# Optimization experiments

Measured on AMD Instinct MI355X. Metric: run time of the kernel, lower is better.

Reference implementation:

```python
import jax, jax.numpy as jnp
import numpy as np

CAPACITY = 0.5  # top_k = int(seq_len * capacity)

def setup_inputs() -> dict:
    key = jax.random.key(0)
    k1, k2, k3, k4 = jax.random.split(key, 4)
    b, s, d, d_ff = 4, 4096, 1024, 4096
    x = jax.random.normal(k1, (b, s, d), dtype=jnp.float32)
    mask = jnp.ones((b, s), dtype=jnp.bool_)
    # learned params: router (Linear(d,1,bias=False)) and the block MLP
    Wr = jax.random.normal(k2, (d, 1), dtype=jnp.float32) * (d ** -0.5)
    W1 = jax.random.normal(k3, (d, d_ff), dtype=jnp.float32) * (d ** -0.5)
    W2 = jax.random.normal(k4, (d_ff, d), dtype=jnp.float32) * (d_ff ** -0.5)
    return {"x": x, "mask": mask, "Wr": Wr, "W1": W1, "W2": W2}

def reference(x, mask, Wr, W1, W2):
    b, s, d = x.shape
    top_k = int(s * CAPACITY)
    # router logits [b, s]
    logits = (x @ Wr)[..., 0]
    # top-k over sequence dim (torch sorted=False; softmax/gather are
    # permutation-equivariant so sorted top_k gives identical results)
    vals, idx = jax.lax.top_k(logits, top_k)          # [b, k]
    order = jnp.argsort(idx, axis=1)                  # sort selected indices ascending
    sel = jnp.take_along_axis(idx, order, axis=1)     # [b, k] token positions, ascending
    w = jax.nn.softmax(vals, axis=1)                  # softmax over selected logits
    r_w = jnp.take_along_axis(w, order, axis=1)       # weights reordered to match sel
    # gather selected tokens
    fx = jnp.take_along_axis(x, sel[..., None], axis=1)  # [b, k, d]
    # block: residual MLP whose update is scaled by router weights (mask unused by MLP)
    h = jax.nn.silu(fx @ W1) @ W2
    out = fx + h * r_w[..., None]
    # scatter processed tokens back into x
    batch = jnp.arange(b)[:, None]
    hidden_states = x.at[batch, sel].set(out)
    # aux loss: faithful to the original (flat view + flat index set, then BCE-with-logits mean)
    flat_logits = logits.reshape(-1)                  # [b*s]
    targets = jnp.zeros_like(flat_logits).at[sel.reshape(-1)].set(1.0)
    aux_loss = jnp.mean(
        jnp.maximum(flat_logits, 0.0)
        - flat_logits * targets
        + jnp.log1p(jnp.exp(-jnp.abs(flat_logits)))
    )
    return hidden_states, aux_loss
```

## Files before the change

kernel.cpp:

```cpp
#include <hip/hip_runtime.h>
#include <hip/hip_bf16.h>
#include <cstdint>

#define B_ 4
#define S_ 4096
#define D_ 1024
#define DFF_ 4096
#define KSEL_ 2048
#define M_ (B_ * KSEL_)
#define NTOK_ (B_ * S_)

typedef short bf16x8 __attribute__((ext_vector_type(8)));
typedef float f32x4 __attribute__((ext_vector_type(4)));

__device__ inline unsigned short f2bf(float f) {
    union { float f; unsigned int u; } c; c.f = f;
    unsigned int u = c.u;
    unsigned int r = u + 0x7fffu + ((u >> 16) & 1u);
    return (unsigned short)(r >> 16);
}

__global__ __launch_bounds__(256)
void transpose_bf16(const float* __restrict__ src, unsigned short* __restrict__ dst,
                    int R, int C) {
    __shared__ float tile[32][33];
    int c0 = blockIdx.x * 32, r0 = blockIdx.y * 32;
    for (int i = threadIdx.y; i < 32; i += 8)
        tile[i][threadIdx.x] = src[(size_t)(r0 + i) * C + c0 + threadIdx.x];
    __syncthreads();
    for (int i = threadIdx.y; i < 32; i += 8)
        dst[(size_t)(c0 + i) * R + r0 + threadIdx.x] = f2bf(tile[threadIdx.x][i]);
}

__global__ __launch_bounds__(256)
void router_kernel(const float* __restrict__ x, const float* __restrict__ Wr,
                   float* __restrict__ logits, unsigned short* __restrict__ xb,
                   float* __restrict__ out) {
    int wid = threadIdx.x >> 6, lane = threadIdx.x & 63;
    int row = blockIdx.x * 4 + wid;
    const float* xr = x + (size_t)row * D_;
    unsigned short* xbr = xb + (size_t)row * D_;
    float* outr = out + (size_t)row * D_;
    float acc = 0.f;
#pragma unroll
    for (int j = 0; j < 4; j++) {
        int off = j * 256 + lane * 4;
        float4 v = *(const float4*)(xr + off);
        float4 w = *(const float4*)(Wr + off);
        acc += v.x * w.x + v.y * w.y + v.z * w.z + v.w * w.w;
        *(float4*)(outr + off) = v;
        ushort4 o;
        o.x = f2bf(v.x); o.y = f2bf(v.y); o.z = f2bf(v.z); o.w = f2bf(v.w);
        *(ushort4*)(xbr + off) = o;
    }
#pragma unroll
    for (int s = 32; s; s >>= 1) acc += __shfl_xor(acc, s);
    if (lane == 0) logits[row] = acc;
}

__global__ __launch_bounds__(256)
void rank_partial_kernel(const float* __restrict__ logits, int* __restrict__ rank) {
    __shared__ float lj[512];
    int b  = blockIdx.x >> 7;
    int ic = (blockIdx.x >> 3) & 15;
    int jc = blockIdx.x & 7;
    const float* L = logits + b * S_;
    for (int t = threadIdx.x; t < 512; t += 256) lj[t] = L[jc * 512 + t];
    __syncthreads();
    int i = ic * 256 + threadIdx.x;
    float li = L[i];
    int jbase = jc * 512;
    int r = 0;
    const float4* __restrict__ lj4 = (const float4*)lj;
#pragma unroll 4
    for (int q = 0; q < 128; q++) {
        float4 v = lj4[q];
        int jb = jbase + q * 4;
        r += (v.x > li) | ((v.x == li) & (jb     < i));
        r += (v.y > li) | ((v.y == li) & (jb + 1 < i));
        r += (v.z > li) | ((v.z == li) & (jb + 2 < i));
        r += (v.w > li) | ((v.w == li) & (jb + 3 < i));
    }
    atomicAdd(&rank[b * S_ + i], r);
}

__global__ __launch_bounds__(256)
void compact_kernel(const float* __restrict__ logits, const int* __restrict__ rank,
                    int* __restrict__ flags,
                    int* __restrict__ rowidx, float* __restrict__ rw) {
    __shared__ float lg[S_];
    __shared__ int f[S_];
    __shared__ int tsum[256];
    __shared__ float red[256];
    int b = blockIdx.x;
    const float* L = logits + b * S_;
    const int* R = rank + b * S_;
    int* F = flags + b * S_;
    for (int j = threadIdx.x; j < S_ / 4; j += 256) {
        ((float4*)lg)[j] = ((const float4*)L)[j];
        int4 rk = ((const int4*)R)[j];
        int4 fl;
        fl.x = rk.x < KSEL_; fl.y = rk.y < KSEL_;
        fl.z = rk.z < KSEL_; fl.w = rk.w < KSEL_;
        ((int4*)f)[j] = fl;
        ((int4*)F)[j] = fl;
    }
    __syncthreads();
    float mx = -INFINITY;
    for (int j = threadIdx.x; j < S_; j += 256) mx = fmaxf(mx, lg[j]);
    red[threadIdx.x] = mx; __syncthreads();
    for (int s = 128; s; s >>= 1) {
        if (threadIdx.x < s) red[threadIdx.x] = fmaxf(red[threadIdx.x], red[threadIdx.x + s]);
        __syncthreads();
    }
    float m = red[0];
    __syncthreads();

    float esum = 0.f;
    int s0 = 0;
#pragma unroll
    for (int j = 0; j < 16; j++) {
        int i = threadIdx.x * 16 + j;
        s0 += f[i];
        if (f[i]) esum += expf(lg[i] - m);
    }
    red[threadIdx.x] = esum; __syncthreads();
    for (int s = 128; s; s >>= 1) {
        if (threadIdx.x < s) red[threadIdx.x] += red[threadIdx.x + s];
        __syncthreads();
    }
    float inv = 1.f / red[0];

    tsum[threadIdx.x] = s0; __syncthreads();
    for (int s = 1; s < 256; s <<= 1) {
        int u = (threadIdx.x >= s) ? tsum[threadIdx.x - s] : 0;
        __syncthreads();
        tsum[threadIdx.x] += u;
        __syncthreads();
    }
    int pos = tsum[threadIdx.x] - s0;
    for (int j = 0; j < 16; j++) {
        int i = threadIdx.x * 16 + j;
        if (f[i]) {
            rowidx[b * KSEL_ + pos] = b * S_ + i;
            rw[b * KSEL_ + pos] = expf(lg[i] - m) * inv;
            pos++;
        }
    }
}

__global__ __launch_bounds__(256)
void loss_kernel(const float* __restrict__ logits, const int* __restrict__ flags,
                 float* __restrict__ partials) {
    __shared__ float red[256];
    int i = blockIdx.x * 256 + threadIdx.x;
    float l = logits[i];
    float t = 0.f;
    if (i < S_)
        t = (flags[i] | flags[S_ + i] | flags[2 * S_ + i] | flags[3 * S_ + i]) ? 1.f : 0.f;
    float v = fmaxf(l, 0.f) - l * t + log1pf(expf(-fabsf(l)));
    red[threadIdx.x] = v; __syncthreads();
    for (int s = 128; s; s >>= 1) {
        if (threadIdx.x < s) red[threadIdx.x] += red[threadIdx.x + s];
        __syncthreads();
    }
    if (threadIdx.x == 0) partials[blockIdx.x] = red[0];
}

__global__ void loss_final(const float* __restrict__ partials, float* __restrict__ out) {
    float v = partials[threadIdx.x];
#pragma unroll
    for (int s = 32; s; s >>= 1) v += __shfl_xor(v, s);
    if (threadIdx.x == 0) out[0] = v / (float)NTOK_;
}

template <int MODE, int N, int K, int SUBS>
__global__ __launch_bounds__(512, 2)
void gemm_pipe_kernel(const unsigned short* __restrict__ A,
                      const unsigned short* __restrict__ BT,
                      const int* __restrict__ rowidx,
                      const float* __restrict__ rw,
                      const float* __restrict__ x,
                      unsigned short* __restrict__ Hout,
                      float* __restrict__ Out) {
    constexpr int BM = 128, BN = 256, BK = 64;
    constexpr int KI = K / BK;
    constexpr int NT = N / BN;
    constexpr int MG = M_ / (BM * SUBS);
    constexpr int NWG = NT * MG;
    constexpr int CPX = NWG / 8;
    __shared__ __attribute__((aligned(16))) unsigned short As[3][BM * BK];
    __shared__ __attribute__((aligned(16))) unsigned short Bs[3][BN * BK];

    const int tid = threadIdx.x;
    const int w = tid >> 6, lane = tid & 63;
    const int wm = w >> 2, wn = w & 3;

    int wgid = blockIdx.y * NT + blockIdx.x;
    int swz = (wgid & 7) * CPX + (wgid >> 3);
    const int tile_n = (swz % NT) * BN;
    const int mgrp   = (swz / NT);

    const int srow = lane >> 3;
    const int sw = (lane & 7) ^ srow;
    const uint64_t abase = (uint64_t)(uintptr_t)A;
    const uint64_t bbase = (uint64_t)(uintptr_t)BT;
    uint64_t aaddr[SUBS][2], baddr[4];
#pragma unroll
    for (int s = 0; s < SUBS; ++s)
#pragma unroll
        for (int t = 0; t < 2; ++t) {
            int r = t * 64 + w * 8 + srow;
            int am = (mgrp * SUBS + s) * BM + r;
            int ar = (MODE == 1) ? rowidx[am] : am;
            aaddr[s][t] = abase + ((uint64_t)ar * K + (uint64_t)sw * 8) * 2ull;
        }
#pragma unroll
    for (int t = 0; t < 4; ++t) {
        int r = t * 64 + w * 8 + srow;
        baddr[t] = bbase + ((uint64_t)(tile_n + r) * K + (uint64_t)sw * 8) * 2ull;
    }

    auto gload = [&](unsigned short* lds, uint64_t gaddr) {
        __builtin_amdgcn_global_load_lds(
            (const __attribute__((address_space(1))) unsigned int*)(uintptr_t)gaddr,
            (__attribute__((address_space(3))) unsigned int*)lds, 16, 0, 0);
    };

    f32x4 acc[4][4];
#pragma unroll
    for (int i = 0; i < 4; i++)
#pragma unroll
        for (int j = 0; j < 4; j++) acc[i][j] = (f32x4){0.f, 0.f, 0.f, 0.f};

#pragma unroll
    for (int p = 0; p < 2; ++p) {
        const uint64_t koff = (uint64_t)p * (BK * 2);
        gload(&As[p][(0 * 64 + w * 8) * BK], aaddr[0][0] + koff);
        gload(&As[p][(1 * 64 + w * 8) * BK], aaddr[0][1] + koff);
#pragma unroll
        for (int t = 0; t < 4; ++t)
            gload(&Bs[p][(t * 64 + w * 8) * BK], baddr[t] + koff);
    }
    asm volatile("s_waitcnt vmcnt(6)" ::: "memory");
    asm volatile("s_barrier" ::: "memory");

    const int lr = lane & 15, quad = lane >> 4;
    int c = 0;
#pragma unroll
    for (int s = 0; s < SUBS; ++s) {
#pragma unroll 1
        for (int kt = 0; kt < KI; ++kt) {
            int pre = c + 2; if (pre >= 3) pre -= 3;
            const char* Abase_l = (const char*)&As[c][0];
            const char* Bbase_l = (const char*)&Bs[c][0];
            const bool cross = (kt + 2 >= KI);
            const bool do_stage = (s < SUBS - 1) || (kt + 2 < KI);
            const uint64_t sa0 = cross ? aaddr[(s + 1 < SUBS) ? s + 1 : s][0]
                                       : aaddr[s][0];
            const uint64_t sa1 = cross ? aaddr[(s + 1 < SUBS) ? s + 1 : s][1]
                                       : aaddr[s][1];
            const uint64_t koff = (uint64_t)((kt + 2) & (KI - 1)) * (BK * 2);

            {
                bf16x8 af[4], bfr[4];
                const int xo = (quad ^ (lr & 7)) * 16;
#pragma unroll
                for (int m4 = 0; m4 < 4; ++m4) {
                    int row = wm * 64 + m4 * 16 + lr;
                    af[m4] = *(const bf16x8*)(Abase_l + row * (BK * 2) + xo);
                }
#pragma unroll
                for (int n4 = 0; n4 < 4; ++n4) {
                    int col = wn * 64 + n4 * 16 + lr;
                    bfr[n4] = *(const bf16x8*)(Bbase_l + col * (BK * 2) + xo);
                }
                if (do_stage) {
                    gload(&As[pre][(0 * 64 + w * 8) * BK], sa0 + koff);
                    gload(&As[pre][(1 * 64 + w * 8) * BK], sa1 + koff);
                    gload(&Bs[pre][(w * 8) * BK], baddr[0] + koff);
                }
                asm volatile("s_barrier" ::: "memory");
                asm volatile("s_waitcnt lgkmcnt(0)" ::: "memory");
                __builtin_amdgcn_sched_barrier(0);
                __builtin_amdgcn_s_setprio(1);
#pragma unroll
                for (int m4 = 0; m4 < 4; ++m4)
#pragma unroll
                    for (int n4 = 0; n4 < 4; ++n4)
                        acc[m4][n4] = __builtin_amdgcn_mfma_f32_16x16x32_bf16(
                            af[m4], bfr[n4], acc[m4][n4], 0, 0, 0);
                __builtin_amdgcn_s_setprio(0);
                asm volatile("s_barrier" ::: "memory");
            }

            {
                bf16x8 af[4], bfr[4];
                const int xo = ((4 + quad) ^ (lr & 7)) * 16;
#pragma unroll
                for (int m4 = 0; m4 < 4; ++m4) {
                    int row = wm * 64 + m4 * 16 + lr;
                    af[m4] = *(const bf16x8*)(Abase_l + row * (BK * 2) + xo);
                }
#pragma unroll
                for (int n4 = 0; n4 < 4; ++n4) {
                    int col = wn * 64 + n4 * 16 + lr;
                    bfr[n4] = *(const bf16x8*)(Bbase_l + col * (BK * 2) + xo);
                }
                if (do_stage) {
#pragma unroll
                    for (int t = 1; t < 4; ++t)
                        gload(&Bs[pre][(t * 64 + w * 8) * BK], baddr[t] + koff);
                }
                asm volatile("s_barrier" ::: "memory");
                asm volatile("s_waitcnt lgkmcnt(0)" ::: "memory");
                __builtin_amdgcn_sched_barrier(0);
                __builtin_amdgcn_s_setprio(1);
#pragma unroll
                for (int m4 = 0; m4 < 4; ++m4)
#pragma unroll
                    for (int n4 = 0; n4 < 4; ++n4)
                        acc[m4][n4] = __builtin_amdgcn_mfma_f32_16x16x32_bf16(
                            af[m4], bfr[n4], acc[m4][n4], 0, 0, 0);
                __builtin_amdgcn_s_setprio(0);
                if (do_stage) {
                    asm volatile("s_waitcnt vmcnt(6)" ::: "memory");
                } else if (kt + 2 == KI) {
                    asm volatile("s_waitcnt vmcnt(0)" ::: "memory");
                }
                asm volatile("s_barrier" ::: "memory");
                c += 1; if (c >= 3) c = 0;
            }
        }

        if (MODE == 1) {
            const int tile_m = (mgrp * SUBS + s) * BM;
#pragma unroll
            for (int m4 = 0; m4 < 4; ++m4)
#pragma unroll
                for (int r = 0; r < 4; ++r) {
                    int m = tile_m + wm * 64 + m4 * 16 + quad * 4 + r;
#pragma unroll
                    for (int n4 = 0; n4 < 4; ++n4) {
                        int col = tile_n + wn * 64 + n4 * 16 + lr;
                        float v = acc[m4][n4][r];
                        v = v / (1.f + __expf(-v));
                        Hout[(uint64_t)m * N + col] = f2bf(v);
                    }
                }
            if (s + 1 < SUBS) {
#pragma unroll
                for (int i = 0; i < 4; i++)
#pragma unroll
                    for (int j = 0; j < 4; j++)
                        acc[i][j] = (f32x4){0.f, 0.f, 0.f, 0.f};
            }
        }
    }

    if (MODE == 2) {
        const int tile_m = mgrp * SUBS * BM;
#pragma unroll
        for (int m4 = 0; m4 < 4; ++m4)
#pragma unroll
            for (int r = 0; r < 4; ++r) {
                int m = tile_m + wm * 64 + m4 * 16 + quad * 4 + r;
                int grow = rowidx[m];
                float wgt = rw[m];
                uint64_t rb = (uint64_t)grow * D_;
#pragma unroll
                for (int n4 = 0; n4 < 4; ++n4) {
                    int col = tile_n + wn * 64 + n4 * 16 + lr;
                    Out[rb + col] = x[rb + col] + acc[m4][n4][r] * wgt;
                }
            }
    }
}

extern "C" void kernel_launch(void* const* d_in, const int* in_sizes, int n_in,
                              void* d_out, int out_size, void* d_ws, size_t ws_size,
                              hipStream_t stream) {
    const float* x  = (const float*)d_in[0];
    const float* Wr = (const float*)d_in[2];
    const float* W1 = (const float*)d_in[3];
    const float* W2 = (const float*)d_in[4];
    float* out = (float*)d_out;

    char* ws = (char*)d_ws;
    size_t off = 0;
    auto alloc = [&](size_t bytes) {
        char* p = ws + off;
        off = (off + bytes + 255) & ~(size_t)255;
        return p;
    };
    unsigned short* xb   = (unsigned short*)alloc((size_t)NTOK_ * D_ * 2);
    unsigned short* W1bT = (unsigned short*)alloc((size_t)DFF_ * D_ * 2);
    unsigned short* W2bT = (unsigned short*)alloc((size_t)D_ * DFF_ * 2);
    unsigned short* H    = (unsigned short*)alloc((size_t)M_ * DFF_ * 2);
    float* logits  = (float*)alloc(NTOK_ * 4);
    int*   rank    = (int*)alloc(NTOK_ * 4);
    int*   flags   = (int*)alloc(NTOK_ * 4);
    int*   rowidx  = (int*)alloc(M_ * 4);
    float* rwp     = (float*)alloc(M_ * 4);
    float* partials = (float*)alloc(64 * 4);

    (void)hipMemsetAsync(rank, 0, NTOK_ * 4, stream);

    transpose_bf16<<<dim3(DFF_ / 32, D_ / 32), dim3(32, 8), 0, stream>>>(W1, W1bT, D_, DFF_);
    transpose_bf16<<<dim3(D_ / 32, DFF_ / 32), dim3(32, 8), 0, stream>>>(W2, W2bT, DFF_, D_);
    router_kernel<<<NTOK_ / 4, 256, 0, stream>>>(x, Wr, logits, xb, out);
    rank_partial_kernel<<<512, 256, 0, stream>>>(logits, rank);
    compact_kernel<<<B_, 256, 0, stream>>>(logits, rank, flags, rowidx, rwp);
    loss_kernel<<<NTOK_ / 256, 256, 0, stream>>>(logits, flags, partials);
    loss_final<<<1, 64, 0, stream>>>(partials, out + (size_t)NTOK_ * D_);
    gemm_pipe_kernel<1, DFF_, D_, 4><<<dim3(DFF_ / 256, M_ / (128 * 4)), 512, 0, stream>>>(
        xb, W1bT, rowidx, nullptr, nullptr, H, nullptr);
    gemm_pipe_kernel<2, D_, DFF_, 1><<<dim3(D_ / 256, M_ / 128), 512, 0, stream>>>(
        H, W2bT, rowidx, rwp, x, nullptr, out);
}
```

Baseline: 355.8 us.

## Add 256x256-tile pipelined GEMM1 kernel and merge small launches

Replaces the first MLP GEMM (gather, W1, SiLU) with a new kernel that uses 256x256 output tiles, BK=32 with a 4-slot LDS ring filled by direct global-to-LDS loads, and interleaves A/B staging with MFMA halves. It also fuses the two weight-transpose launches into one and the two-stage loss reduction into a single-block kernel. The aim is more operand reuse per tile and fewer kernel launches. In exchange, register pressure from the 8x4 accumulator array is higher, the tile count per GPU shrinks, and the single-block loss kernel serializes its work.

```diff
diff --git a/kernel.cpp b/kernel.cpp
--- a/kernel.cpp
+++ b/kernel.cpp
@@ -21,10 +21,20 @@
 }
 
 __global__ __launch_bounds__(256)
-void transpose_bf16(const float* __restrict__ src, unsigned short* __restrict__ dst,
-                    int R, int C) {
+void transpose2_bf16(const float* __restrict__ W1, unsigned short* __restrict__ W1bT,
+                     const float* __restrict__ W2, unsigned short* __restrict__ W2bT) {
     __shared__ float tile[32][33];
-    int c0 = blockIdx.x * 32, r0 = blockIdx.y * 32;
+    int id = blockIdx.x;
+    const float* src; unsigned short* dst; int R, C, bx, by;
+    if (id < (DFF_ / 32) * (D_ / 32)) {
+        src = W1; dst = W1bT; R = D_; C = DFF_;
+        bx = id % (DFF_ / 32); by = id / (DFF_ / 32);
+    } else {
+        id -= (DFF_ / 32) * (D_ / 32);
+        src = W2; dst = W2bT; R = DFF_; C = D_;
+        bx = id % (D_ / 32); by = id / (D_ / 32);
+    }
+    int c0 = bx * 32, r0 = by * 32;
     for (int i = threadIdx.y; i < 32; i += 8)
         tile[i][threadIdx.x] = src[(size_t)(r0 + i) * C + c0 + threadIdx.x];
     __syncthreads();
@@ -149,29 +159,188 @@
     }
 }
 
-__global__ __launch_bounds__(256)
-void loss_kernel(const float* __restrict__ logits, const int* __restrict__ flags,
-                 float* __restrict__ partials) {
-    __shared__ float red[256];
-    int i = blockIdx.x * 256 + threadIdx.x;
-    float l = logits[i];
-    float t = 0.f;
-    if (i < S_)
-        t = (flags[i] | flags[S_ + i] | flags[2 * S_ + i] | flags[3 * S_ + i]) ? 1.f : 0.f;
-    float v = fmaxf(l, 0.f) - l * t + log1pf(expf(-fabsf(l)));
-    red[threadIdx.x] = v; __syncthreads();
-    for (int s = 128; s; s >>= 1) {
+__global__ __launch_bounds__(1024)
+void loss_fused(const float* __restrict__ logits, const int* __restrict__ flags,
+                float* __restrict__ out) {
+    __shared__ float red[1024];
+    float acc = 0.f;
+    for (int i = threadIdx.x; i < NTOK_; i += 1024) {
+        float l = logits[i];
+        float t = 0.f;
+        if (i < S_)
+            t = (flags[i] | flags[S_ + i] | flags[2 * S_ + i] | flags[3 * S_ + i]) ? 1.f : 0.f;
+        acc += fmaxf(l, 0.f) - l * t + log1pf(expf(-fabsf(l)));
+    }
+    red[threadIdx.x] = acc; __syncthreads();
+    for (int s = 512; s; s >>= 1) {
         if (threadIdx.x < s) red[threadIdx.x] += red[threadIdx.x + s];
         __syncthreads();
     }
-    if (threadIdx.x == 0) partials[blockIdx.x] = red[0];
-}
-
-__global__ void loss_final(const float* __restrict__ partials, float* __restrict__ out) {
-    float v = partials[threadIdx.x];
-#pragma unroll
-    for (int s = 32; s; s >>= 1) v += __shfl_xor(v, s);
-    if (threadIdx.x == 0) out[0] = v / (float)NTOK_;
+    if (threadIdx.x == 0) out[0] = red[0] / (float)NTOK_;
+}
+
+template <int N, int K, int SUBS>
+__global__ __launch_bounds__(512, 2)
+void gemm1_256_kernel(const unsigned short* __restrict__ A,
+                      const unsigned short* __restrict__ BT,
+                      const int* __restrict__ rowidx,
+                      unsigned short* __restrict__ Hout) {
+    static_assert(SUBS == 2, "address selection hardcoded for SUBS=2");
+    constexpr int BKS = 32;
+    constexpr int NSUB = K / BKS;
+    constexpr int NSTEPS = SUBS * NSUB;
+    constexpr int NT = N / 256;
+    constexpr int MG = M_ / (256 * SUBS);
+    constexpr int NWG = NT * MG;
+    constexpr int CPX = NWG / 8;
+    __shared__ __attribute__((aligned(16))) unsigned short As[4][256 * BKS];
+    __shared__ __attribute__((aligned(16))) unsigned short Bs[4][256 * BKS];
+
+    const int tid = threadIdx.x;
+    const int w = tid >> 6, lane = tid & 63;
+    const int wm = w >> 2, wn = w & 3;
+
+    int wgid = blockIdx.y * NT + blockIdx.x;
+    int swz = (wgid & 7) * CPX + (wgid >> 3);
+    const int tile_n = (swz % NT) * 256;
+    const int mgrp   = swz / NT;
+
+    const int srow = tid >> 2;
+    const int lchunk = (tid & 3) ^ ((tid >> 3) & 3);
+    const uint64_t abase = (uint64_t)(uintptr_t)A;
+    const uint64_t bbase = (uint64_t)(uintptr_t)BT;
+    uint64_t aaddr[SUBS][2], baddr[2];
+#pragma unroll
+    for (int s = 0; s < SUBS; ++s)
+#pragma unroll
+        for (int i = 0; i < 2; ++i) {
+            int r = i * 128 + srow;
+            int ar = rowidx[(mgrp * SUBS + s) * 256 + r];
+            aaddr[s][i] = abase + ((uint64_t)ar * K + (uint64_t)lchunk * 8) * 2ull;
+        }
+#pragma unroll
+    for (int i = 0; i < 2; ++i) {
+        int r = i * 128 + srow;
+        baddr[i] = bbase + ((uint64_t)(tile_n + r) * K + (uint64_t)lchunk * 8) * 2ull;
+    }
+
+    auto gload = [&](unsigned short* lds, uint64_t gaddr) {
+        __builtin_amdgcn_global_load_lds(
+            (const __attribute__((address_space(1))) unsigned int*)(uintptr_t)gaddr,
+            (__attribute__((address_space(3))) unsigned int*)lds, 16, 0, 0);
+    };
+    auto stageA = [&](int g, int slot) {
+        const uint64_t koff = (uint64_t)(g & (NSUB - 1)) * (BKS * 2);
+        const uint64_t a0 = (g >= NSUB) ? aaddr[1][0] : aaddr[0][0];
+        const uint64_t a1 = (g >= NSUB) ? aaddr[1][1] : aaddr[0][1];
+        gload(&As[slot][(0 * 512 + w * 64) * 8], a0 + koff);
+        gload(&As[slot][(1 * 512 + w * 64) * 8], a1 + koff);
+    };
+    auto stageB = [&](int g, int slot) {
+        const uint64_t koff = (uint64_t)(g & (NSUB - 1)) * (BKS * 2);
+        gload(&Bs[slot][(0 * 512 + w * 64) * 8], baddr[0] + koff);
+        gload(&Bs[slot][(1 * 512 + w * 64) * 8], baddr[1] + koff);
+    };
+
+    f32x4 acc[8][4];
+#pragma unroll
+    for (int i = 0; i < 8; i++)
+#pragma unroll
+        for (int j = 0; j < 4; j++) acc[i][j] = (f32x4){0.f, 0.f, 0.f, 0.f};
+
+    const int lr = lane & 15, quad = lane >> 4;
+    const int xo = (quad ^ ((lr >> 1) & 3)) * 16;
+
+    auto flush = [&](int s) {
+        const int tm = (mgrp * SUBS + s) * 256 + wm * 128;
+#pragma unroll
+        for (int m4 = 0; m4 < 8; ++m4)
+#pragma unroll
+            for (int r = 0; r < 4; ++r) {
+                int m = tm + m4 * 16 + quad * 4 + r;
+#pragma unroll
+                for (int n4 = 0; n4 < 4; ++n4) {
+                    int col = tile_n + wn * 64 + n4 * 16 + lr;
+                    float v = acc[m4][n4][r];
+                    v = v / (1.f + __expf(-v));
+                    Hout[(uint64_t)m * N + col] = f2bf(v);
+                }
+            }
+    };
+
+    stageA(0, 0); stageB(0, 0);
+    stageA(1, 1); stageB(1, 1);
+    stageA(2, 2); stageB(2, 2);
+    asm volatile("s_waitcnt vmcnt(8)" ::: "memory");
+    asm volatile("s_barrier" ::: "memory");
+
+#pragma unroll 1
+    for (int t = 0; t < NSTEPS; ++t) {
+        const int c = t & 3, pslot = (t + 3) & 3;
+        const bool dost = (t + 3 < NSTEPS);
+        const char* Ab = (const char*)&As[c][0];
+        const char* Bb = (const char*)&Bs[c][0];
+
+        bf16x8 bfr[4];
+        {
+            bf16x8 af[4];
+#pragma unroll
+            for (int m4 = 0; m4 < 4; ++m4)
+                af[m4] = *(const bf16x8*)(Ab + (wm * 128 + m4 * 16 + lr) * 64 + xo);
+#pragma unroll
+            for (int n4 = 0; n4 < 4; ++n4)
+                bfr[n4] = *(const bf16x8*)(Bb + (wn * 64 + n4 * 16 + lr) * 64 + xo);
+            if (dost) stageA(t + 3, pslot);
+            asm volatile("s_barrier" ::: "memory");
+            asm volatile("s_waitcnt lgkmcnt(0)" ::: "memory");
+            __builtin_amdgcn_sched_barrier(0);
+            __builtin_amdgcn_s_setprio(1);
+#pragma unroll
+            for (int m4 = 0; m4 < 4; ++m4)
+#pragma unroll
+                for (int n4 = 0; n4 < 4; ++n4)
+                    acc[m4][n4] = __builtin_amdgcn_mfma_f32_16x16x32_bf16(
+                        af[m4], bfr[n4], acc[m4][n4], 0, 0, 0);
+            __builtin_amdgcn_s_setprio(0);
+            asm volatile("s_barrier" ::: "memory");
+        }
+
+        {
+            bf16x8 af[4];
+#pragma unroll
+            for (int m4 = 0; m4 < 4; ++m4)
+                af[m4] = *(const bf16x8*)(Ab + (wm * 128 + 64 + m4 * 16 + lr) * 64 + xo);
+            if (dost) stageB(t + 3, pslot);
+            asm volatile("s_barrier" ::: "memory");
+            asm volatile("s_waitcnt lgkmcnt(0)" ::: "memory");
+            __builtin_amdgcn_sched_barrier(0);
+            __builtin_amdgcn_s_setprio(1);
+#pragma unroll
+            for (int m4 = 0; m4 < 4; ++m4)
+#pragma unroll
+                for (int n4 = 0; n4 < 4; ++n4)
+                    acc[4 + m4][n4] = __builtin_amdgcn_mfma_f32_16x16x32_bf16(
+                        af[m4], bfr[n4], acc[4 + m4][n4], 0, 0, 0);
+            __builtin_amdgcn_s_setprio(0);
+            if (t + 3 < NSTEPS) {
+                asm volatile("s_waitcnt vmcnt(8)" ::: "memory");
+            } else if (t + 2 < NSTEPS) {
+                asm volatile("s_waitcnt vmcnt(4)" ::: "memory");
+            } else if (t + 1 < NSTEPS) {
+                asm volatile("s_waitcnt vmcnt(0)" ::: "memory");
+            }
+            asm volatile("s_barrier" ::: "memory");
+        }
+
+        if ((t & (NSUB - 1)) == (NSUB - 1) && (t + 1) < NSTEPS) {
+            flush(t / NSUB);
+#pragma unroll
+            for (int i = 0; i < 8; i++)
+#pragma unroll
+                for (int j = 0; j < 4; j++) acc[i][j] = (f32x4){0.f, 0.f, 0.f, 0.f};
+        }
+    }
+    flush(SUBS - 1);
 }
 
 template <int MODE, int N, int K, int SUBS>
@@ -402,19 +571,17 @@
     int*   flags   = (int*)alloc(NTOK_ * 4);
     int*   rowidx  = (int*)alloc(M_ * 4);
     float* rwp     = (float*)alloc(M_ * 4);
-    float* partials = (float*)alloc(64 * 4);
 
     (void)hipMemsetAsync(rank, 0, NTOK_ * 4, stream);
 
-    transpose_bf16<<<dim3(DFF_ / 32, D_ / 32), dim3(32, 8), 0, stream>>>(W1, W1bT, D_, DFF_);
-    transpose_bf16<<<dim3(D_ / 32, DFF_ / 32), dim3(32, 8), 0, stream>>>(W2, W2bT, DFF_, D_);
+    transpose2_bf16<<<2 * (DFF_ / 32) * (D_ / 32), dim3(32, 8), 0, stream>>>(
+        W1, W1bT, W2, W2bT);
     router_kernel<<<NTOK_ / 4, 256, 0, stream>>>(x, Wr, logits, xb, out);
     rank_partial_kernel<<<512, 256, 0, stream>>>(logits, rank);
     compact_kernel<<<B_, 256, 0, stream>>>(logits, rank, flags, rowidx, rwp);
-    loss_kernel<<<NTOK_ / 256, 256, 0, stream>>>(logits, flags, partials);
-    loss_final<<<1, 64, 0, stream>>>(partials, out + (size_t)NTOK_ * D_);
-    gemm_pipe_kernel<1, DFF_, D_, 4><<<dim3(DFF_ / 256, M_ / (128 * 4)), 512, 0, stream>>>(
-        xb, W1bT, rowidx, nullptr, nullptr, H, nullptr);
+    loss_fused<<<1, 1024, 0, stream>>>(logits, flags, out + (size_t)NTOK_ * D_);
+    gemm1_256_kernel<DFF_, D_, 2><<<dim3(DFF_ / 256, M_ / 512), 512, 0, stream>>>(
+        xb, W1bT, rowidx, H);
     gemm_pipe_kernel<2, D_, DFF_, 1><<<dim3(D_ / 256, M_ / 128), 512, 0, stream>>>(
         H, W2bT, rowidx, rwp, x, nullptr, out);
 }
```

New measurement: 363.4 us. 2.1% more time.

## Fuse pre-GEMM kernels into one cooperative kernel with grid syncs

Applied to the files above, without the earlier changes.

Replaces the memset, two weight transposes, router, rank, compact and loss kernels with a single cooperative kernel of 256 blocks of 1024 threads that uses grid.sync between phases. The weight transposes are overlapped with the compact phase by running them on the blocks not doing compaction. This removes several launch gaps and the memset. In exchange it adds grid-wide barriers and forces fewer, larger blocks, which may lower occupancy in the bandwidth-bound router and transpose phases.

```diff
diff --git a/kernel.cpp b/kernel.cpp
--- a/kernel.cpp
+++ b/kernel.cpp
@@ -1,6 +1,9 @@
 #include <hip/hip_runtime.h>
 #include <hip/hip_bf16.h>
+#include <hip/hip_cooperative_groups.h>
 #include <cstdint>
+
+namespace cg = cooperative_groups;
 
 #define B_ 4
 #define S_ 4096
@@ -20,158 +23,195 @@
     return (unsigned short)(r >> 16);
 }
 
-__global__ __launch_bounds__(256)
-void transpose_bf16(const float* __restrict__ src, unsigned short* __restrict__ dst,
-                    int R, int C) {
-    __shared__ float tile[32][33];
-    int c0 = blockIdx.x * 32, r0 = blockIdx.y * 32;
-    for (int i = threadIdx.y; i < 32; i += 8)
-        tile[i][threadIdx.x] = src[(size_t)(r0 + i) * C + c0 + threadIdx.x];
-    __syncthreads();
-    for (int i = threadIdx.y; i < 32; i += 8)
-        dst[(size_t)(c0 + i) * R + r0 + threadIdx.x] = f2bf(tile[threadIdx.x][i]);
-}
-
-__global__ __launch_bounds__(256)
-void router_kernel(const float* __restrict__ x, const float* __restrict__ Wr,
-                   float* __restrict__ logits, unsigned short* __restrict__ xb,
-                   float* __restrict__ out) {
-    int wid = threadIdx.x >> 6, lane = threadIdx.x & 63;
-    int row = blockIdx.x * 4 + wid;
-    const float* xr = x + (size_t)row * D_;
-    unsigned short* xbr = xb + (size_t)row * D_;
-    float* outr = out + (size_t)row * D_;
-    float acc = 0.f;
-#pragma unroll
-    for (int j = 0; j < 4; j++) {
-        int off = j * 256 + lane * 4;
-        float4 v = *(const float4*)(xr + off);
-        float4 w = *(const float4*)(Wr + off);
-        acc += v.x * w.x + v.y * w.y + v.z * w.z + v.w * w.w;
-        *(float4*)(outr + off) = v;
-        ushort4 o;
-        o.x = f2bf(v.x); o.y = f2bf(v.y); o.z = f2bf(v.z); o.w = f2bf(v.w);
-        *(ushort4*)(xbr + off) = o;
-    }
-#pragma unroll
-    for (int s = 32; s; s >>= 1) acc += __shfl_xor(acc, s);
-    if (lane == 0) logits[row] = acc;
-}
-
-__global__ __launch_bounds__(256)
-void rank_partial_kernel(const float* __restrict__ logits, int* __restrict__ rank) {
-    __shared__ float lj[512];
-    int b  = blockIdx.x >> 7;
-    int ic = (blockIdx.x >> 3) & 15;
-    int jc = blockIdx.x & 7;
-    const float* L = logits + b * S_;
-    for (int t = threadIdx.x; t < 512; t += 256) lj[t] = L[jc * 512 + t];
-    __syncthreads();
-    int i = ic * 256 + threadIdx.x;
-    float li = L[i];
-    int jbase = jc * 512;
-    int r = 0;
-    const float4* __restrict__ lj4 = (const float4*)lj;
+__global__ __launch_bounds__(1024)
+void fused_pre(const float* __restrict__ x, const float* __restrict__ Wr,
+               const float* __restrict__ W1, const float* __restrict__ W2,
+               float* __restrict__ logits, int* __restrict__ rank,
+               int* __restrict__ flags, int* __restrict__ rowidx,
+               float* __restrict__ rw, unsigned short* __restrict__ xb,
+               float* __restrict__ out, unsigned short* __restrict__ W1bT,
+               unsigned short* __restrict__ W2bT, float* __restrict__ partials,
+               float* __restrict__ lossout) {
+    cg::grid_group grid = cg::this_grid();
+    const int tid = threadIdx.x;
+
+    __shared__ float sh_lg[S_];
+    __shared__ int   sh_f[S_];
+    __shared__ int   sh_tsum[1024];
+    __shared__ float sh_red[1024];
+    __shared__ float sh_tile[4][32][33];
+    __shared__ float sh_lj[2][512];
+
+    {
+        int zi = blockIdx.x * 1024 + tid;
+        if (zi < NTOK_) rank[zi] = 0;
+
+        int gw = blockIdx.x * 16 + (tid >> 6);
+        int lane = tid & 63;
+        for (int row = gw; row < NTOK_; row += 4096) {
+            const float* xr = x + (size_t)row * D_;
+            unsigned short* xbr = xb + (size_t)row * D_;
+            float* outr = out + (size_t)row * D_;
+            float acc = 0.f;
+#pragma unroll
+            for (int j = 0; j < 4; j++) {
+                int off = j * 256 + lane * 4;
+                float4 v = *(const float4*)(xr + off);
+                float4 wv = *(const float4*)(Wr + off);
+                acc += v.x * wv.x + v.y * wv.y + v.z * wv.z + v.w * wv.w;
+                *(float4*)(outr + off) = v;
+                ushort4 o;
+                o.x = f2bf(v.x); o.y = f2bf(v.y); o.z = f2bf(v.z); o.w = f2bf(v.w);
+                *(ushort4*)(xbr + off) = o;
+            }
+#pragma unroll
+            for (int s = 32; s; s >>= 1) acc += __shfl_xor(acc, s);
+            if (lane == 0) logits[row] = acc;
+        }
+    }
+    grid.sync();
+
+    {
+        int g = tid >> 8;
+        int lt = tid & 255;
+        int b = 0, ic = 0, jc = 0;
+        if (g < 2) {
+            int vb = blockIdx.x * 2 + g;
+            b = vb >> 7; ic = (vb >> 3) & 15; jc = vb & 7;
+            const float* L = logits + b * S_;
+            for (int t = lt; t < 512; t += 256) sh_lj[g][t] = L[jc * 512 + t];
+        }
+        __syncthreads();
+        if (g < 2) {
+            const float* L = logits + b * S_;
+            int i = ic * 256 + lt;
+            float li = L[i];
+            int jbase = jc * 512;
+            int r = 0;
+            const float4* lj4 = (const float4*)sh_lj[g];
 #pragma unroll 4
-    for (int q = 0; q < 128; q++) {
-        float4 v = lj4[q];
-        int jb = jbase + q * 4;
-        r += (v.x > li) | ((v.x == li) & (jb     < i));
-        r += (v.y > li) | ((v.y == li) & (jb + 1 < i));
-        r += (v.z > li) | ((v.z == li) & (jb + 2 < i));
-        r += (v.w > li) | ((v.w == li) & (jb + 3 < i));
-    }
-    atomicAdd(&rank[b * S_ + i], r);
-}
-
-__global__ __launch_bounds__(256)
-void compact_kernel(const float* __restrict__ logits, const int* __restrict__ rank,
-                    int* __restrict__ flags,
-                    int* __restrict__ rowidx, float* __restrict__ rw) {
-    __shared__ float lg[S_];
-    __shared__ int f[S_];
-    __shared__ int tsum[256];
-    __shared__ float red[256];
-    int b = blockIdx.x;
-    const float* L = logits + b * S_;
-    const int* R = rank + b * S_;
-    int* F = flags + b * S_;
-    for (int j = threadIdx.x; j < S_ / 4; j += 256) {
-        ((float4*)lg)[j] = ((const float4*)L)[j];
-        int4 rk = ((const int4*)R)[j];
-        int4 fl;
-        fl.x = rk.x < KSEL_; fl.y = rk.y < KSEL_;
-        fl.z = rk.z < KSEL_; fl.w = rk.w < KSEL_;
-        ((int4*)f)[j] = fl;
-        ((int4*)F)[j] = fl;
-    }
-    __syncthreads();
-    float mx = -INFINITY;
-    for (int j = threadIdx.x; j < S_; j += 256) mx = fmaxf(mx, lg[j]);
-    red[threadIdx.x] = mx; __syncthreads();
-    for (int s = 128; s; s >>= 1) {
-        if (threadIdx.x < s) red[threadIdx.x] = fmaxf(red[threadIdx.x], red[threadIdx.x + s]);
+            for (int q = 0; q < 128; q++) {
+                float4 v = lj4[q];
+                int jb = jbase + q * 4;
+                r += (v.x > li) | ((v.x == li) & (jb     < i));
+                r += (v.y > li) | ((v.y == li) & (jb + 1 < i));
+                r += (v.z > li) | ((v.z == li) & (jb + 2 < i));
+                r += (v.w > li) | ((v.w == li) & (jb + 3 < i));
+            }
+            atomicAdd(&rank[b * S_ + i], r);
+        }
+    }
+    grid.sync();
+
+    if (blockIdx.x < 4) {
+        int b = blockIdx.x;
+        const float* L = logits + b * S_;
+        const int* R = rank + b * S_;
+        int* F = flags + b * S_;
+        {
+            ((float4*)sh_lg)[tid] = ((const float4*)L)[tid];
+            int4 rk = ((const int4*)R)[tid];
+            int4 fl;
+            fl.x = rk.x < KSEL_; fl.y = rk.y < KSEL_;
+            fl.z = rk.z < KSEL_; fl.w = rk.w < KSEL_;
+            ((int4*)sh_f)[tid] = fl;
+            ((int4*)F)[tid] = fl;
+        }
         __syncthreads();
-    }
-    float m = red[0];
-    __syncthreads();
-
-    float esum = 0.f;
-    int s0 = 0;
-#pragma unroll
-    for (int j = 0; j < 16; j++) {
-        int i = threadIdx.x * 16 + j;
-        s0 += f[i];
-        if (f[i]) esum += expf(lg[i] - m);
-    }
-    red[threadIdx.x] = esum; __syncthreads();
-    for (int s = 128; s; s >>= 1) {
-        if (threadIdx.x < s) red[threadIdx.x] += red[threadIdx.x + s];
+        float mx = fmaxf(fmaxf(sh_lg[tid * 4], sh_lg[tid * 4 + 1]),
+                         fmaxf(sh_lg[tid * 4 + 2], sh_lg[tid * 4 + 3]));
+        sh_red[tid] = mx; __syncthreads();
+        for (int s = 512; s; s >>= 1) {
+            if (tid < s) sh_red[tid] = fmaxf(sh_red[tid], sh_red[tid + s]);
+            __syncthreads();
+        }
+        float m = sh_red[0];
         __syncthreads();
-    }
-    float inv = 1.f / red[0];
-
-    tsum[threadIdx.x] = s0; __syncthreads();
-    for (int s = 1; s < 256; s <<= 1) {
-        int u = (threadIdx.x >= s) ? tsum[threadIdx.x - s] : 0;
-        __syncthreads();
-        tsum[threadIdx.x] += u;
-        __syncthreads();
-    }
-    int pos = tsum[threadIdx.x] - s0;
-    for (int j = 0; j < 16; j++) {
-        int i = threadIdx.x * 16 + j;
-        if (f[i]) {
-            rowidx[b * KSEL_ + pos] = b * S_ + i;
-            rw[b * KSEL_ + pos] = expf(lg[i] - m) * inv;
-            pos++;
-        }
-    }
-}
-
-__global__ __launch_bounds__(256)
-void loss_kernel(const float* __restrict__ logits, const int* __restrict__ flags,
-                 float* __restrict__ partials) {
-    __shared__ float red[256];
-    int i = blockIdx.x * 256 + threadIdx.x;
-    float l = logits[i];
-    float t = 0.f;
-    if (i < S_)
-        t = (flags[i] | flags[S_ + i] | flags[2 * S_ + i] | flags[3 * S_ + i]) ? 1.f : 0.f;
-    float v = fmaxf(l, 0.f) - l * t + log1pf(expf(-fabsf(l)));
-    red[threadIdx.x] = v; __syncthreads();
-    for (int s = 128; s; s >>= 1) {
-        if (threadIdx.x < s) red[threadIdx.x] += red[threadIdx.x + s];
-        __syncthreads();
-    }
-    if (threadIdx.x == 0) partials[blockIdx.x] = red[0];
-}
-
-__global__ void loss_final(const float* __restrict__ partials, float* __restrict__ out) {
-    float v = partials[threadIdx.x];
-#pragma unroll
-    for (int s = 32; s; s >>= 1) v += __shfl_xor(v, s);
-    if (threadIdx.x == 0) out[0] = v / (float)NTOK_;
+        float esum = 0.f;
+        int s0 = 0;
+#pragma unroll
+        for (int j = 0; j < 4; j++) {
+            int i = tid * 4 + j;
+            s0 += sh_f[i];
+            if (sh_f[i]) esum += expf(sh_lg[i] - m);
+        }
+        sh_red[tid] = esum; __syncthreads();
+        for (int s = 512; s; s >>= 1) {
+            if (tid < s) sh_red[tid] += sh_red[tid + s];
+            __syncthreads();
+        }
+        float inv = 1.f / sh_red[0];
+        sh_tsum[tid] = s0; __syncthreads();
+        for (int s = 1; s < 1024; s <<= 1) {
+            int u = (tid >= s) ? sh_tsum[tid - s] : 0;
+            __syncthreads();
+            sh_tsum[tid] += u;
+            __syncthreads();
+        }
+        int pos = sh_tsum[tid] - s0;
+#pragma unroll
+        for (int j = 0; j < 4; j++) {
+            int i = tid * 4 + j;
+            if (sh_f[i]) {
+                rowidx[b * KSEL_ + pos] = b * S_ + i;
+                rw[b * KSEL_ + pos] = expf(sh_lg[i] - m) * inv;
+                pos++;
+            }
+        }
+    } else {
+        int group = tid >> 8;
+        int tx = tid & 31, ty = (tid >> 5) & 7;
+        const int TILES = 2 * (DFF_ / 32) * (D_ / 32);
+        for (int it = 0; it < 9; ++it) {
+            int tile = (blockIdx.x - 4) * 4 + group + it * 1008;
+            bool ok = tile < TILES;
+            const float* src = nullptr; unsigned short* dst = nullptr;
+            int R = 0, C = 0, bx = 0, by = 0;
+            if (ok) {
+                if (tile < (DFF_ / 32) * (D_ / 32)) {
+                    src = W1; dst = W1bT; R = D_; C = DFF_;
+                    bx = tile % (DFF_ / 32); by = tile / (DFF_ / 32);
+                } else {
+                    int t2 = tile - (DFF_ / 32) * (D_ / 32);
+                    src = W2; dst = W2bT; R = DFF_; C = D_;
+                    bx = t2 % (D_ / 32); by = t2 / (D_ / 32);
+                }
+                int c0 = bx * 32, r0 = by * 32;
+                for (int i = ty; i < 32; i += 8)
+                    sh_tile[group][i][tx] = src[(size_t)(r0 + i) * C + c0 + tx];
+            }
+            __syncthreads();
+            if (ok) {
+                int c0 = bx * 32, r0 = by * 32;
+                for (int i = ty; i < 32; i += 8)
+                    dst[(size_t)(c0 + i) * R + r0 + tx] = f2bf(sh_tile[group][tx][i]);
+            }
+            __syncthreads();
+        }
+    }
+    grid.sync();
+
+    if (blockIdx.x < 16) {
+        int i = blockIdx.x * 1024 + tid;
+        float l = logits[i];
+        float t = 0.f;
+        if (i < S_)
+            t = (flags[i] | flags[S_ + i] | flags[2 * S_ + i] | flags[3 * S_ + i]) ? 1.f : 0.f;
+        float v = fmaxf(l, 0.f) - l * t + log1pf(expf(-fabsf(l)));
+        sh_red[tid] = v; __syncthreads();
+        for (int s = 512; s; s >>= 1) {
+            if (tid < s) sh_red[tid] += sh_red[tid + s];
+            __syncthreads();
+        }
+        if (tid == 0) partials[blockIdx.x] = sh_red[0];
+    }
+    grid.sync();
+    if (blockIdx.x == 0 && tid < 64) {
+        float v = (tid < 16) ? partials[tid] : 0.f;
+#pragma unroll
+        for (int s = 32; s; s >>= 1) v += __shfl_xor(v, s);
+        if (tid == 0) lossout[0] = v / (float)NTOK_;
+    }
 }
 
 template <int MODE, int N, int K, int SUBS>
@@ -402,17 +442,18 @@
     int*   flags   = (int*)alloc(NTOK_ * 4);
     int*   rowidx  = (int*)alloc(M_ * 4);
     float* rwp     = (float*)alloc(M_ * 4);
-    float* partials = (float*)alloc(64 * 4);
-
-    (void)hipMemsetAsync(rank, 0, NTOK_ * 4, stream);
-
-    transpose_bf16<<<dim3(DFF_ / 32, D_ / 32), dim3(32, 8), 0, stream>>>(W1, W1bT, D_, DFF_);
-    transpose_bf16<<<dim3(D_ / 32, DFF_ / 32), dim3(32, 8), 0, stream>>>(W2, W2bT, DFF_, D_);
-    router_kernel<<<NTOK_ / 4, 256, 0, stream>>>(x, Wr, logits, xb, out);
-    rank_partial_kernel<<<512, 256, 0, stream>>>(logits, rank);
-    compact_kernel<<<B_, 256, 0, stream>>>(logits, rank, flags, rowidx, rwp);
-    loss_kernel<<<NTOK_ / 256, 256, 0, stream>>>(logits, flags, partials);
-    loss_final<<<1, 64, 0, stream>>>(partials, out + (size_t)NTOK_ * D_);
+    float* partials = (float*)alloc(16 * 4);
+    float* lossp = out + (size_t)NTOK_ * D_;
+
+    void* kargs[] = {
+        (void*)&x, (void*)&Wr, (void*)&W1, (void*)&W2,
+        (void*)&logits, (void*)&rank, (void*)&flags, (void*)&rowidx,
+        (void*)&rwp, (void*)&xb, (void*)&out, (void*)&W1bT, (void*)&W2bT,
+        (void*)&partials, (void*)&lossp
+    };
+    (void)hipLaunchCooperativeKernel((const void*)fused_pre, dim3(256),
+                                     dim3(1024), kargs, 0, stream);
+
     gemm_pipe_kernel<1, DFF_, D_, 4><<<dim3(DFF_ / 256, M_ / (128 * 4)), 512, 0, stream>>>(
         xb, W1bT, rowidx, nullptr, nullptr, H, nullptr);
     gemm_pipe_kernel<2, D_, DFF_, 1><<<dim3(D_ / 256, M_ / 128), 512, 0, stream>>>(
```

Result: slower. 485.5 us (+36.4%).
